# Kernel optimization log

Hardware: AMD Instinct MI355X
Metric: run time of the kernel (lower is better)

## Reference

```python
import jax, jax.numpy as jnp
import numpy as np
import math

HEADS, IN_DIM, OUT_DIM, N = 8, 256, 64, 4096

def _glorot(key, shape):
    fan = shape[-2] + shape[-1]
    lim = math.sqrt(6.0 / fan)
    return jax.random.uniform(key, shape, jnp.float32, -lim, lim)

def setup_inputs() -> dict:
    key = jax.random.key(0)
    ks = jax.random.split(key, 6)
    return {
        "input_x": jax.random.normal(ks[0], (N, IN_DIM), jnp.float32),
        "WQ": _glorot(ks[1], (HEADS, IN_DIM, OUT_DIM)),
        "WK": _glorot(ks[2], (HEADS, IN_DIM, OUT_DIM)),
        "WV": _glorot(ks[3], (HEADS, IN_DIM, OUT_DIM)),
        "lin_w": _glorot(ks[4], (OUT_DIM, HEADS * OUT_DIM)),
        "lin_b": jnp.zeros((OUT_DIM,), jnp.float32),
    }

def reference(input_x, WQ, WK, WV, lin_w, lin_b):
    # Q,K,V: [H, N, D] via broadcasted matmul of [N,in] @ [H,in,D]
    Q = jnp.einsum('ni,hid->hnd', input_x, WQ)
    K = jnp.einsum('ni,hid->hnd', input_x, WK)
    V = jnp.einsum('ni,hid->hnd', input_x, WV)
    scores = jnp.einsum('hnd,hmd->hnm', Q, K)  # [H, N, N]
    # Original adds diag_embed(diag(scores) - 1e20): diagonal -> 2*orig - 1e20
    idx = jnp.arange(scores.shape[-1])
    scores = scores.at[:, idx, idx].add(scores[:, idx, idx] - 1e20)
    attn = jax.nn.softmax(scores / math.sqrt(OUT_DIM), axis=-1)
    attn_x = jnp.einsum('hnm,hmd->hnd', attn, V)  # [H, N, D]
    # cat heads along feature dim: [N, H*D]
    attn_cat = jnp.transpose(attn_x, (1, 0, 2)).reshape(attn_x.shape[1], -1)
    return attn_cat @ lin_w.T + lin_b
```

## Files before the change

kernel.cpp:

```cpp
#include <hip/hip_runtime.h>
#include <hip/hip_bf16.h>

#define SEQ  4096
#define HEADS 8
#define IND  256
#define OUTD 64
#define NSPLIT 4
#define QBLK 128
#define TILES_PER_SLICE (SEQ / 64 / NSPLIT)

typedef __attribute__((ext_vector_type(8))) short bf16x8;
typedef __attribute__((ext_vector_type(4))) float f32x4;

__device__ __forceinline__ unsigned short f2bf(float f) {
  union { __hip_bfloat16 h; unsigned short u; } c;
  c.h = __float2bfloat16(f);
  return c.u;
}
__device__ __forceinline__ float bf2f(unsigned short u) {
  union { unsigned u; float f; } c;
  c.u = ((unsigned)u) << 16;
  return c.f;
}
__device__ __forceinline__ float fast_exp2(float x) {
#if __has_builtin(__builtin_amdgcn_exp2f)
  return __builtin_amdgcn_exp2f(x);
#else
  float r;
  asm("v_exp_f32 %0, %1" : "=v"(r) : "v"(x));
  return r;
#endif
}
__device__ __forceinline__ unsigned pk2(float hi, float lo) {
  return __builtin_amdgcn_perm(__builtin_bit_cast(unsigned, hi),
                               __builtin_bit_cast(unsigned, lo), 0x07060302u);
}
__device__ __forceinline__ int pcol(int k) {
  return (k >> 5) * 32 + ((k >> 2) & 3) * 8 + ((k >> 4) & 1) * 4 + (k & 3);
}

__global__ void prep_kernel(const float* __restrict__ WQ,
                            const float* __restrict__ WK,
                            const float* __restrict__ WV,
                            const float* __restrict__ LW,
                            unsigned short* __restrict__ WTQ,
                            unsigned short* __restrict__ WTK,
                            unsigned short* __restrict__ WTV,
                            unsigned short* __restrict__ LWB) {
  const int NW = HEADS * IND * OUTD;
  const int NL = OUTD * HEADS * OUTD;
  int i = blockIdx.x * 256 + threadIdx.x;
  if (i < 3 * NW) {
    int which = i / NW;
    int r = i % NW;
    int h = r / (IND * OUTD);
    int rem = r % (IND * OUTD);
    int d = rem / IND;
    int ii = rem % IND;
    const float* W = (which == 0) ? WQ : ((which == 1) ? WK : WV);
    float v = W[(h * IND + ii) * OUTD + d];
    if (which == 0) v *= 0.125f * 1.44269504088896f;
    unsigned short* DST = (which == 0) ? WTQ : ((which == 1) ? WTK : WTV);
    DST[h * OUTD * IND + d * IND + ii] = f2bf(v);
  } else if (i < 3 * NW + NL) {
    int k = i - 3 * NW;
    LWB[k] = f2bf(LW[k]);
  }
}

__global__ __launch_bounds__(256) void proj_kernel(
    const float* __restrict__ X,
    const unsigned short* __restrict__ WTQ,
    const unsigned short* __restrict__ WTK,
    const unsigned short* __restrict__ WTV,
    unsigned short* __restrict__ Qo,
    unsigned short* __restrict__ KS,
    unsigned short* __restrict__ VS) {
  const int tb = blockIdx.x;
  const int h  = blockIdx.y;

  __shared__ unsigned short Xl[64 * 72];
  __shared__ unsigned short Wl[3][64 * 72];

  const int tid = threadIdx.x;
  const int lane = tid & 63;
  const int w = tid >> 6;
  const int m16 = lane & 15;
  const int g = lane >> 4;

  const unsigned short* W0 = WTQ + h * OUTD * IND;
  const unsigned short* W1 = WTK + h * OUTD * IND;
  const unsigned short* W2 = WTV + h * OUTD * IND;

  f32x4 acc[3][4];
#pragma unroll
  for (int z = 0; z < 3; ++z)
#pragma unroll
    for (int ns = 0; ns < 4; ++ns) {
      f32x4 z4 = {0.f, 0.f, 0.f, 0.f};
      acc[z][ns] = z4;
    }

  for (int kb = 0; kb < 4; ++kb) {
    if (kb) __syncthreads();
    for (int s = tid; s < 512; s += 256) {
      int row = s >> 3, sg = s & 7;
      const float* xs = X + (size_t)(tb * 64 + row) * IND + kb * 64 + sg * 8;
      float4 x0 = *(const float4*)xs;
      float4 x1 = *(const float4*)(xs + 4);
      uint4 u;
      u.x = ((unsigned)f2bf(x0.y) << 16) | f2bf(x0.x);
      u.y = ((unsigned)f2bf(x0.w) << 16) | f2bf(x0.z);
      u.z = ((unsigned)f2bf(x1.y) << 16) | f2bf(x1.x);
      u.w = ((unsigned)f2bf(x1.w) << 16) | f2bf(x1.z);
      *(uint4*)(&Xl[row * 72 + sg * 8]) = u;
      *(uint4*)(&Wl[0][row * 72 + sg * 8]) =
          *(const uint4*)(W0 + (size_t)row * IND + kb * 64 + sg * 8);
      *(uint4*)(&Wl[1][row * 72 + sg * 8]) =
          *(const uint4*)(W1 + (size_t)row * IND + kb * 64 + sg * 8);
      *(uint4*)(&Wl[2][row * 72 + sg * 8]) =
          *(const uint4*)(W2 + (size_t)row * IND + kb * 64 + sg * 8);
    }
    __syncthreads();
    bf16x8 xa0 = *(const bf16x8*)(&Xl[(w * 16 + m16) * 72 + g * 8]);
    bf16x8 xa1 = *(const bf16x8*)(&Xl[(w * 16 + m16) * 72 + 32 + g * 8]);
#pragma unroll
    for (int z = 0; z < 2; ++z)
#pragma unroll
      for (int ns = 0; ns < 4; ++ns) {
        bf16x8 b0 = *(const bf16x8*)(&Wl[z][(ns * 16 + m16) * 72 + g * 8]);
        bf16x8 b1 = *(const bf16x8*)(&Wl[z][(ns * 16 + m16) * 72 + 32 + g * 8]);
        acc[z][ns] = __builtin_amdgcn_mfma_f32_16x16x32_bf16(xa0, b0, acc[z][ns], 0, 0, 0);
        acc[z][ns] = __builtin_amdgcn_mfma_f32_16x16x32_bf16(xa1, b1, acc[z][ns], 0, 0, 0);
      }
    bf16x8 wa0 = *(const bf16x8*)(&Wl[2][(w * 16 + m16) * 72 + g * 8]);
    bf16x8 wa1 = *(const bf16x8*)(&Wl[2][(w * 16 + m16) * 72 + 32 + g * 8]);
#pragma unroll
    for (int ns = 0; ns < 4; ++ns) {
      bf16x8 b0 = *(const bf16x8*)(&Xl[(ns * 16 + m16) * 72 + g * 8]);
      bf16x8 b1 = *(const bf16x8*)(&Xl[(ns * 16 + m16) * 72 + 32 + g * 8]);
      acc[2][ns] = __builtin_amdgcn_mfma_f32_16x16x32_bf16(wa0, b0, acc[2][ns], 0, 0, 0);
      acc[2][ns] = __builtin_amdgcn_mfma_f32_16x16x32_bf16(wa1, b1, acc[2][ns], 0, 0, 0);
    }
  }
#pragma unroll
  for (int ns = 0; ns < 4; ++ns)
#pragma unroll
    for (int r = 0; r < 4; ++r) {
      int token = tb * 64 + w * 16 + 4 * g + r;
      int d = ns * 16 + m16;
      Qo[(size_t)h * SEQ * OUTD + (size_t)token * OUTD + d] = f2bf(acc[0][ns][r]);
    }
  {
    unsigned short* O = KS + ((size_t)(h * 64 + tb)) * 4096;
#pragma unroll
    for (int ns = 0; ns < 4; ++ns)
#pragma unroll
      for (int r = 0; r < 4; ++r) {
        int rk = w * 16 + 4 * g + r;
        int d = ns * 16 + m16;
        int c = d >> 3;
        int idx = rk * 64 + ((c ^ (rk & 7)) << 3) + (d & 7);
        O[idx] = f2bf(acc[1][ns][r]);
      }
  }
  {
    unsigned short* O = VS + ((size_t)(h * 64 + tb)) * 4096;
#pragma unroll
    for (int ns = 0; ns < 4; ++ns) {
      int cp = pcol(ns * 16 + m16);
      int c = cp >> 3, j = cp & 7;
#pragma unroll
      for (int r = 0; r < 4; ++r) {
        int rv = w * 16 + 4 * g + r;
        int idx = rv * 64 + ((c ^ (rv & 7)) << 3) + j;
        O[idx] = f2bf(acc[2][ns][r]);
      }
    }
  }
}

__global__ __launch_bounds__(256, 4) void attn_kernel(
    const unsigned short* __restrict__ Q,
    const unsigned short* __restrict__ KS,
    const unsigned short* __restrict__ VS,
    unsigned short* __restrict__ PART,
    float* __restrict__ L) {
  const int qb = blockIdx.x;
  const int h  = blockIdx.y;
  const int sl = blockIdx.z;
  const int kb0 = sl * TILES_PER_SLICE;
  const unsigned short* Qh = Q + (size_t)h * SEQ * OUTD;

  __shared__ unsigned short Kl[3][4096];
  __shared__ unsigned short Vl[2][4096];

  const int tid = threadIdx.x;
  const int lane = tid & 63;
  const int w = tid >> 6;
  const int m16 = lane & 15;
  const int g = lane >> 4;
  const int e = m16 & 7;
  const int c0s = ((g ^ e) << 3);
  const int c1s = (((g + 4) ^ e) << 3);

  const int qrowA = qb * QBLK + w * 16 + m16;
  const int qrowB = qrowA + 64;
  bf16x8 qfA0 = *(const bf16x8*)(Qh + (size_t)qrowA * OUTD + g * 8);
  bf16x8 qfA1 = *(const bf16x8*)(Qh + (size_t)qrowA * OUTD + 32 + g * 8);
  bf16x8 qfB0 = *(const bf16x8*)(Qh + (size_t)qrowB * OUTD + g * 8);
  bf16x8 qfB1 = *(const bf16x8*)(Qh + (size_t)qrowB * OUTD + 32 + g * 8);

  f32x4 accA[4], accB[4], acc5A, acc5B;
#pragma unroll
  for (int s4 = 0; s4 < 4; ++s4) {
    f32x4 z4 = {0.f, 0.f, 0.f, 0.f};
    accA[s4] = z4; accB[s4] = z4;
  }
  { f32x4 z4 = {0.f, 0.f, 0.f, 0.f}; acc5A = z4; acc5B = z4; }
  const f32x4 zero4 = {0.f, 0.f, 0.f, 0.f};
  bf16x8 ones;
#pragma unroll
  for (int j = 0; j < 8; ++j) ones[j] = (short)0x3F80;

  const unsigned short* kg = KS + ((size_t)(h * 64 + kb0)) * 4096 + w * 512 + lane * 8;
  const unsigned short* vg = VS + ((size_t)(h * 64 + kb0)) * 4096 + w * 512 + lane * 8;

  auto stageK = [&](int buf) {
    __builtin_amdgcn_global_load_lds(kg, &Kl[buf][w * 512], 16, 0, 0);
    __builtin_amdgcn_global_load_lds(kg + 2048, &Kl[buf][2048 + w * 512], 16, 0, 0);
    kg += 4096;
  };
  auto stageV = [&](int buf) {
    __builtin_amdgcn_global_load_lds(vg, &Vl[buf][w * 512], 16, 0, 0);
    __builtin_amdgcn_global_load_lds(vg + 2048, &Vl[buf][2048 + w * 512], 16, 0, 0);
    vg += 4096;
  };

  stageK(0);
  stageV(0);
  stageK(1);
  asm volatile("s_waitcnt vmcnt(2)" ::: "memory");
  __builtin_amdgcn_s_barrier();
  asm volatile("" ::: "memory");

#pragma unroll
  for (int it = 0; it < TILES_PER_SLICE; ++it) {
    const int kb = kb0 + it;
    const int kcur = it % 3;
    const int vcur = it & 1;
    if (it + 1 < TILES_PER_SLICE) stageV((it + 1) & 1);
    if (it + 2 < TILES_PER_SLICE) stageK((it + 2) % 3);

    f32x4 stA[4], stB[4];
    __builtin_amdgcn_s_setprio(1);
#pragma unroll
    for (int t = 0; t < 4; ++t) {
      const unsigned short* krow = &Kl[kcur][(t * 16 + m16) * 64];
      bf16x8 ka0 = *(const bf16x8*)(krow + c0s);
      bf16x8 ka1 = *(const bf16x8*)(krow + c1s);
      stA[t] = __builtin_amdgcn_mfma_f32_16x16x32_bf16(ka0, qfA0, zero4, 0, 0, 0);
      stA[t] = __builtin_amdgcn_mfma_f32_16x16x32_bf16(ka1, qfA1, stA[t], 0, 0, 0);
      stB[t] = __builtin_amdgcn_mfma_f32_16x16x32_bf16(ka0, qfB0, zero4, 0, 0, 0);
      stB[t] = __builtin_amdgcn_mfma_f32_16x16x32_bf16(ka1, qfB1, stB[t], 0, 0, 0);
    }
    __builtin_amdgcn_s_setprio(0);

    if (kb == 2 * qb) {
#pragma unroll
      for (int t = 0; t < 4; ++t)
#pragma unroll
        for (int r = 0; r < 4; ++r)
          if (t == w && (4 * g + r) == m16) stA[t][r] = -1e30f;
    }
    if (kb == 2 * qb + 1) {
#pragma unroll
      for (int t = 0; t < 4; ++t)
#pragma unroll
        for (int r = 0; r < 4; ++r)
          if (t == w && (4 * g + r) == m16) stB[t][r] = -1e30f;
    }

    float eA[16], eB[16];
#pragma unroll
    for (int t = 0; t < 4; ++t)
#pragma unroll
      for (int r = 0; r < 4; ++r) {
        eA[t * 4 + r] = fast_exp2(stA[t][r]);
        eB[t * 4 + r] = fast_exp2(stB[t][r]);
      }
    uint4 uA0, uA1, uB0, uB1;
    uA0.x = pk2(eA[1], eA[0]);   uA0.y = pk2(eA[3], eA[2]);
    uA0.z = pk2(eA[5], eA[4]);   uA0.w = pk2(eA[7], eA[6]);
    uA1.x = pk2(eA[9], eA[8]);   uA1.y = pk2(eA[11], eA[10]);
    uA1.z = pk2(eA[13], eA[12]); uA1.w = pk2(eA[15], eA[14]);
    uB0.x = pk2(eB[1], eB[0]);   uB0.y = pk2(eB[3], eB[2]);
    uB0.z = pk2(eB[5], eB[4]);   uB0.w = pk2(eB[7], eB[6]);
    uB1.x = pk2(eB[9], eB[8]);   uB1.y = pk2(eB[11], eB[10]);
    uB1.z = pk2(eB[13], eB[12]); uB1.w = pk2(eB[15], eB[14]);
    bf16x8 pbA0 = __builtin_bit_cast(bf16x8, uA0);
    bf16x8 pbA1 = __builtin_bit_cast(bf16x8, uA1);
    bf16x8 pbB0 = __builtin_bit_cast(bf16x8, uB0);
    bf16x8 pbB1 = __builtin_bit_cast(bf16x8, uB1);

    __builtin_amdgcn_s_setprio(1);
#pragma unroll
    for (int s4 = 0; s4 < 4; ++s4) {
      const unsigned short* vrow = &Vl[vcur][(s4 * 16 + m16) * 64];
      bf16x8 va0 = *(const bf16x8*)(vrow + c0s);
      bf16x8 va1 = *(const bf16x8*)(vrow + c1s);
      accA[s4] = __builtin_amdgcn_mfma_f32_16x16x32_bf16(va0, pbA0, accA[s4], 0, 0, 0);
      accA[s4] = __builtin_amdgcn_mfma_f32_16x16x32_bf16(va1, pbA1, accA[s4], 0, 0, 0);
      accB[s4] = __builtin_amdgcn_mfma_f32_16x16x32_bf16(va0, pbB0, accB[s4], 0, 0, 0);
      accB[s4] = __builtin_amdgcn_mfma_f32_16x16x32_bf16(va1, pbB1, accB[s4], 0, 0, 0);
    }
    acc5A = __builtin_amdgcn_mfma_f32_16x16x32_bf16(ones, pbA0, acc5A, 0, 0, 0);
    acc5A = __builtin_amdgcn_mfma_f32_16x16x32_bf16(ones, pbA1, acc5A, 0, 0, 0);
    acc5B = __builtin_amdgcn_mfma_f32_16x16x32_bf16(ones, pbB0, acc5B, 0, 0, 0);
    acc5B = __builtin_amdgcn_mfma_f32_16x16x32_bf16(ones, pbB1, acc5B, 0, 0, 0);
    __builtin_amdgcn_s_setprio(0);

    if (it < TILES_PER_SLICE - 1) {
      if (it < TILES_PER_SLICE - 2) {
        asm volatile("s_waitcnt vmcnt(2)" ::: "memory");
      } else {
        asm volatile("s_waitcnt vmcnt(0)" ::: "memory");
      }
      __builtin_amdgcn_s_barrier();
      asm volatile("" ::: "memory");
    }
  }

  const size_t baseA = (((size_t)sl * HEADS + h) * SEQ + qrowA) * OUTD;
  const size_t baseB = (((size_t)sl * HEADS + h) * SEQ + qrowB) * OUTD;
#pragma unroll
  for (int s4 = 0; s4 < 4; ++s4) {
    uint2 pkA, pkB;
    pkA.x = pk2(accA[s4][1], accA[s4][0]);
    pkA.y = pk2(accA[s4][3], accA[s4][2]);
    pkB.x = pk2(accB[s4][1], accB[s4][0]);
    pkB.y = pk2(accB[s4][3], accB[s4][2]);
    *(uint2*)(&PART[baseA + s4 * 16 + 4 * g]) = pkA;
    *(uint2*)(&PART[baseB + s4 * 16 + 4 * g]) = pkB;
  }
  if (g == 0) {
    L[((size_t)sl * HEADS + h) * SEQ + qrowA] = acc5A[0];
    L[((size_t)sl * HEADS + h) * SEQ + qrowB] = acc5B[0];
  }
}

__global__ __launch_bounds__(128) void final_kernel(
    const unsigned short* __restrict__ PART, const float* __restrict__ L,
    const unsigned short* __restrict__ LWB, const float* __restrict__ LB,
    float* __restrict__ OUT) {
  __shared__ float Rl[64 * 20];
  const int q0 = blockIdx.x * 16;
  const int tid = threadIdx.x;
  const int wv = tid >> 6, lane = tid & 63;
  const int m16 = lane & 15, g = lane >> 4;

  f32x4 acc[4];
#pragma unroll
  for (int ns = 0; ns < 4; ++ns) { f32x4 z4 = {0.f, 0.f, 0.f, 0.f}; acc[ns] = z4; }

#pragma unroll
  for (int kbi = 0; kbi < 4; ++kbi) {
    const int kb = wv * 4 + kbi;
    float lsum = 0.f;
#pragma unroll
    for (int s2 = 0; s2 < NSPLIT; ++s2)
      lsum += L[((size_t)s2 * HEADS + kb) * SEQ + q0 + m16];
    float inv = 1.f / lsum;
    float va[8], vb[8];
#pragma unroll
    for (int j = 0; j < 8; ++j) { va[j] = 0.f; vb[j] = 0.f; }
#pragma unroll
    for (int s2 = 0; s2 < NSPLIT; ++s2) {
      const unsigned short* p =
          PART + (((size_t)s2 * HEADS + kb) * SEQ + q0 + m16) * OUTD;
      bf16x8 t0 = *(const bf16x8*)(p + g * 8);
      bf16x8 t1 = *(const bf16x8*)(p + 32 + g * 8);
#pragma unroll
      for (int j = 0; j < 8; ++j) {
        va[j] += bf2f((unsigned short)t0[j]);
        vb[j] += bf2f((unsigned short)t1[j]);
      }
    }
    uint4 u0, u1;
    u0.x = pk2(va[1] * inv, va[0] * inv); u0.y = pk2(va[3] * inv, va[2] * inv);
    u0.z = pk2(va[5] * inv, va[4] * inv); u0.w = pk2(va[7] * inv, va[6] * inv);
    u1.x = pk2(vb[1] * inv, vb[0] * inv); u1.y = pk2(vb[3] * inv, vb[2] * inv);
    u1.z = pk2(vb[5] * inv, vb[4] * inv); u1.w = pk2(vb[7] * inv, vb[6] * inv);
    bf16x8 a0 = __builtin_bit_cast(bf16x8, u0);
    bf16x8 a1 = __builtin_bit_cast(bf16x8, u1);
#pragma unroll
    for (int ns = 0; ns < 4; ++ns) {
      const unsigned short* lw = LWB + (size_t)(ns * 16 + m16) * 512 + kb * 64;
      bf16x8 b0 = *(const bf16x8*)(lw + g * 8);
      bf16x8 b1 = *(const bf16x8*)(lw + 32 + g * 8);
      acc[ns] = __builtin_amdgcn_mfma_f32_16x16x32_bf16(a0, b0, acc[ns], 0, 0, 0);
      acc[ns] = __builtin_amdgcn_mfma_f32_16x16x32_bf16(a1, b1, acc[ns], 0, 0, 0);
    }
  }

  if (wv == 1) {
#pragma unroll
    for (int ns = 0; ns < 4; ++ns)
      *(f32x4*)(&Rl[lane * 20 + ns * 4]) = acc[ns];
  }
  __syncthreads();
  if (wv == 0) {
#pragma unroll
    for (int ns = 0; ns < 4; ++ns) {
      f32x4 o = acc[ns] + *(const f32x4*)(&Rl[lane * 20 + ns * 4]);
      float b = LB[ns * 16 + m16];
#pragma unroll
      for (int r = 0; r < 4; ++r)
        OUT[(size_t)(q0 + 4 * g + r) * OUTD + ns * 16 + m16] = o[r] + b;
    }
  }
}

extern "C" void kernel_launch(void* const* d_in, const int* in_sizes, int n_in,
                              void* d_out, int out_size, void* d_ws, size_t ws_size,
                              hipStream_t stream) {
  const float* X  = (const float*)d_in[0];
  const float* WQ = (const float*)d_in[1];
  const float* WK = (const float*)d_in[2];
  const float* WV = (const float*)d_in[3];
  const float* LW = (const float*)d_in[4];
  const float* LB = (const float*)d_in[5];

  char* ws = (char*)d_ws;
  unsigned short* Qb  = (unsigned short*)ws;
  unsigned short* KS  = Qb + (size_t)HEADS * SEQ * OUTD;
  unsigned short* VS  = KS + (size_t)HEADS * SEQ * OUTD;
  unsigned short* LWB = VS + (size_t)HEADS * SEQ * OUTD;
  char* region2 = (char*)(LWB + (size_t)OUTD * HEADS * OUTD);

  unsigned short* WTQ = (unsigned short*)region2;
  unsigned short* WTK = WTQ + (size_t)HEADS * OUTD * IND;
  unsigned short* WTV = WTK + (size_t)HEADS * OUTD * IND;

  unsigned short* PART = (unsigned short*)region2;
  float* Lml = (float*)(region2 + (size_t)NSPLIT * HEADS * SEQ * OUTD * 2);

  const int total_prep = 3 * HEADS * IND * OUTD + OUTD * HEADS * OUTD;
  prep_kernel<<<(total_prep + 255) / 256, 256, 0, stream>>>(
      WQ, WK, WV, LW, WTQ, WTK, WTV, LWB);
  proj_kernel<<<dim3(64, 8), 256, 0, stream>>>(X, WTQ, WTK, WTV, Qb, KS, VS);
  attn_kernel<<<dim3(SEQ / QBLK, 8, NSPLIT), 256, 0, stream>>>(Qb, KS, VS, PART, Lml);
  final_kernel<<<256, 128, 0, stream>>>(PART, Lml, LWB, LB, (float*)d_out);
}
```

Measured before the change: 66.29 us.

## Software-pipeline QK and PV across tiles; widen final kernel to four waves

The attention loop is restructured so that each iteration's QK MFMAs are issued alongside the previous tile's PV MFMAs, with exp/pack moved after them and the last PV step peeled out of the loop. The aim is to overlap the exp/transcendental work with matrix-core work instead of serialising them. V staging is shifted by one tile to match the new ordering. The final kernel also moves from two to four waves per block, each handling two heads, with a three-way LDS reduction. This adds register pressure from the live P fragments across iterations and changes the timing of the waits.

```diff
diff --git a/kernel.cpp b/kernel.cpp
--- a/kernel.cpp
+++ b/kernel.cpp
@@ -237,22 +237,10 @@
     vg += 4096;
   };
 
-  stageK(0);
-  stageV(0);
-  stageK(1);
-  asm volatile("s_waitcnt vmcnt(2)" ::: "memory");
-  __builtin_amdgcn_s_barrier();
-  asm volatile("" ::: "memory");
-
-#pragma unroll
-  for (int it = 0; it < TILES_PER_SLICE; ++it) {
-    const int kb = kb0 + it;
-    const int kcur = it % 3;
-    const int vcur = it & 1;
-    if (it + 1 < TILES_PER_SLICE) stageV((it + 1) & 1);
-    if (it + 2 < TILES_PER_SLICE) stageK((it + 2) % 3);
-
-    f32x4 stA[4], stB[4];
+  bf16x8 pbA0, pbA1, pbB0, pbB1;
+  f32x4 stA[4], stB[4];
+
+  auto qk_mfma = [&](int kcur) {
     __builtin_amdgcn_s_setprio(1);
 #pragma unroll
     for (int t = 0; t < 4; ++t) {
@@ -265,22 +253,42 @@
       stB[t] = __builtin_amdgcn_mfma_f32_16x16x32_bf16(ka1, qfB1, stB[t], 0, 0, 0);
     }
     __builtin_amdgcn_s_setprio(0);
-
-    if (kb == 2 * qb) {
+  };
+
+  auto pv_step = [&](int vbuf) {
+    __builtin_amdgcn_s_setprio(1);
+#pragma unroll
+    for (int s4 = 0; s4 < 4; ++s4) {
+      const unsigned short* vrow = &Vl[vbuf][(s4 * 16 + m16) * 64];
+      bf16x8 va0 = *(const bf16x8*)(vrow + c0s);
+      bf16x8 va1 = *(const bf16x8*)(vrow + c1s);
+      accA[s4] = __builtin_amdgcn_mfma_f32_16x16x32_bf16(va0, pbA0, accA[s4], 0, 0, 0);
+      accA[s4] = __builtin_amdgcn_mfma_f32_16x16x32_bf16(va1, pbA1, accA[s4], 0, 0, 0);
+      accB[s4] = __builtin_amdgcn_mfma_f32_16x16x32_bf16(va0, pbB0, accB[s4], 0, 0, 0);
+      accB[s4] = __builtin_amdgcn_mfma_f32_16x16x32_bf16(va1, pbB1, accB[s4], 0, 0, 0);
+    }
+    acc5A = __builtin_amdgcn_mfma_f32_16x16x32_bf16(ones, pbA0, acc5A, 0, 0, 0);
+    acc5A = __builtin_amdgcn_mfma_f32_16x16x32_bf16(ones, pbA1, acc5A, 0, 0, 0);
+    acc5B = __builtin_amdgcn_mfma_f32_16x16x32_bf16(ones, pbB0, acc5B, 0, 0, 0);
+    acc5B = __builtin_amdgcn_mfma_f32_16x16x32_bf16(ones, pbB1, acc5B, 0, 0, 0);
+    __builtin_amdgcn_s_setprio(0);
+  };
+
+  auto mask_pack = [&](int kbg) {
+    if (kbg == 2 * qb) {
 #pragma unroll
       for (int t = 0; t < 4; ++t)
 #pragma unroll
         for (int r = 0; r < 4; ++r)
           if (t == w && (4 * g + r) == m16) stA[t][r] = -1e30f;
     }
-    if (kb == 2 * qb + 1) {
+    if (kbg == 2 * qb + 1) {
 #pragma unroll
       for (int t = 0; t < 4; ++t)
 #pragma unroll
         for (int r = 0; r < 4; ++r)
           if (t == w && (4 * g + r) == m16) stB[t][r] = -1e30f;
     }
-
     float eA[16], eB[16];
 #pragma unroll
     for (int t = 0; t < 4; ++t)
@@ -298,27 +306,27 @@
     uB0.z = pk2(eB[5], eB[4]);   uB0.w = pk2(eB[7], eB[6]);
     uB1.x = pk2(eB[9], eB[8]);   uB1.y = pk2(eB[11], eB[10]);
     uB1.z = pk2(eB[13], eB[12]); uB1.w = pk2(eB[15], eB[14]);
-    bf16x8 pbA0 = __builtin_bit_cast(bf16x8, uA0);
-    bf16x8 pbA1 = __builtin_bit_cast(bf16x8, uA1);
-    bf16x8 pbB0 = __builtin_bit_cast(bf16x8, uB0);
-    bf16x8 pbB1 = __builtin_bit_cast(bf16x8, uB1);
-
-    __builtin_amdgcn_s_setprio(1);
-#pragma unroll
-    for (int s4 = 0; s4 < 4; ++s4) {
-      const unsigned short* vrow = &Vl[vcur][(s4 * 16 + m16) * 64];
-      bf16x8 va0 = *(const bf16x8*)(vrow + c0s);
-      bf16x8 va1 = *(const bf16x8*)(vrow + c1s);
-      accA[s4] = __builtin_amdgcn_mfma_f32_16x16x32_bf16(va0, pbA0, accA[s4], 0, 0, 0);
-      accA[s4] = __builtin_amdgcn_mfma_f32_16x16x32_bf16(va1, pbA1, accA[s4], 0, 0, 0);
-      accB[s4] = __builtin_amdgcn_mfma_f32_16x16x32_bf16(va0, pbB0, accB[s4], 0, 0, 0);
-      accB[s4] = __builtin_amdgcn_mfma_f32_16x16x32_bf16(va1, pbB1, accB[s4], 0, 0, 0);
-    }
-    acc5A = __builtin_amdgcn_mfma_f32_16x16x32_bf16(ones, pbA0, acc5A, 0, 0, 0);
-    acc5A = __builtin_amdgcn_mfma_f32_16x16x32_bf16(ones, pbA1, acc5A, 0, 0, 0);
-    acc5B = __builtin_amdgcn_mfma_f32_16x16x32_bf16(ones, pbB0, acc5B, 0, 0, 0);
-    acc5B = __builtin_amdgcn_mfma_f32_16x16x32_bf16(ones, pbB1, acc5B, 0, 0, 0);
-    __builtin_amdgcn_s_setprio(0);
+    pbA0 = __builtin_bit_cast(bf16x8, uA0);
+    pbA1 = __builtin_bit_cast(bf16x8, uA1);
+    pbB0 = __builtin_bit_cast(bf16x8, uB0);
+    pbB1 = __builtin_bit_cast(bf16x8, uB1);
+  };
+
+  stageK(0);
+  stageK(1);
+  asm volatile("s_waitcnt vmcnt(2)" ::: "memory");
+  __builtin_amdgcn_s_barrier();
+  asm volatile("" ::: "memory");
+
+#pragma unroll
+  for (int it = 0; it < TILES_PER_SLICE; ++it) {
+    if (it < TILES_PER_SLICE) stageV(it & 1);
+    if (it + 2 < TILES_PER_SLICE) stageK((it + 2) % 3);
+
+    qk_mfma(it % 3);
+    if (it > 0) pv_step((it - 1) & 1);
+
+    mask_pack(kb0 + it);
 
     if (it < TILES_PER_SLICE - 1) {
       if (it < TILES_PER_SLICE - 2) {
@@ -330,6 +338,10 @@
       asm volatile("" ::: "memory");
     }
   }
+  asm volatile("s_waitcnt vmcnt(0)" ::: "memory");
+  __builtin_amdgcn_s_barrier();
+  asm volatile("" ::: "memory");
+  pv_step((TILES_PER_SLICE - 1) & 1);
 
   const size_t baseA = (((size_t)sl * HEADS + h) * SEQ + qrowA) * OUTD;
   const size_t baseB = (((size_t)sl * HEADS + h) * SEQ + qrowB) * OUTD;
@@ -349,11 +361,11 @@
   }
 }
 
-__global__ __launch_bounds__(128) void final_kernel(
+__global__ __launch_bounds__(256) void final_kernel(
     const unsigned short* __restrict__ PART, const float* __restrict__ L,
     const unsigned short* __restrict__ LWB, const float* __restrict__ LB,
     float* __restrict__ OUT) {
-  __shared__ float Rl[64 * 20];
+  __shared__ float Rl[3][64 * 20];
   const int q0 = blockIdx.x * 16;
   const int tid = threadIdx.x;
   const int wv = tid >> 6, lane = tid & 63;
@@ -364,8 +376,8 @@
   for (int ns = 0; ns < 4; ++ns) { f32x4 z4 = {0.f, 0.f, 0.f, 0.f}; acc[ns] = z4; }
 
 #pragma unroll
-  for (int kbi = 0; kbi < 4; ++kbi) {
-    const int kb = wv * 4 + kbi;
+  for (int kbi = 0; kbi < 2; ++kbi) {
+    const int kb = wv * 2 + kbi;
     float lsum = 0.f;
 #pragma unroll
     for (int s2 = 0; s2 < NSPLIT; ++s2)
@@ -403,16 +415,19 @@
     }
   }
 
-  if (wv == 1) {
+  if (wv != 0) {
 #pragma unroll
     for (int ns = 0; ns < 4; ++ns)
-      *(f32x4*)(&Rl[lane * 20 + ns * 4]) = acc[ns];
+      *(f32x4*)(&Rl[wv - 1][lane * 20 + ns * 4]) = acc[ns];
   }
   __syncthreads();
   if (wv == 0) {
 #pragma unroll
     for (int ns = 0; ns < 4; ++ns) {
-      f32x4 o = acc[ns] + *(const f32x4*)(&Rl[lane * 20 + ns * 4]);
+      f32x4 o = acc[ns];
+#pragma unroll
+      for (int rr = 0; rr < 3; ++rr)
+        o += *(const f32x4*)(&Rl[rr][lane * 20 + ns * 4]);
       float b = LB[ns * 16 + m16];
 #pragma unroll
       for (int r = 0; r < 4; ++r)
@@ -450,5 +465,5 @@
       WQ, WK, WV, LW, WTQ, WTK, WTV, LWB);
   proj_kernel<<<dim3(64, 8), 256, 0, stream>>>(X, WTQ, WTK, WTV, Qb, KS, VS);
   attn_kernel<<<dim3(SEQ / QBLK, 8, NSPLIT), 256, 0, stream>>>(Qb, KS, VS, PART, Lml);
-  final_kernel<<<256, 128, 0, stream>>>(PART, Lml, LWB, LB, (float*)d_out);
-}
+  final_kernel<<<256, 256, 0, stream>>>(PART, Lml, LWB, LB, (float*)d_out);
+}
```

After: 67.89 us. +2.4%, slower.

## Split attention warps across query and key halves with LDS reduction, three KV slices

Applied to the files above, without the earlier changes.

Restructures the attention kernel so each warp pair covers 64 query rows and half of each 64-key tile. This lets the ones-vector MFMA row-sum be replaced by a VALU sum of bf16-truncated exponentials. The two key halves are reduced through LDS at the end, and the KV split drops from 4 to 3 uneven slices (22/21/21 tiles) with launch bounds lowered to 3. The aim is to cut redundant MFMA work and fit the grid to the CU count, at the cost of an extra LDS reduction and a non-unrolled loop.

```diff
diff --git a/kernel.cpp b/kernel.cpp
--- a/kernel.cpp
+++ b/kernel.cpp
@@ -5,9 +5,8 @@
 #define HEADS 8
 #define IND  256
 #define OUTD 64
-#define NSPLIT 4
+#define NSPLIT 3
 #define QBLK 128
-#define TILES_PER_SLICE (SEQ / 64 / NSPLIT)
 
 typedef __attribute__((ext_vector_type(8))) short bf16x8;
 typedef __attribute__((ext_vector_type(4))) float f32x4;
@@ -30,6 +29,9 @@
   asm("v_exp_f32 %0, %1" : "=v"(r) : "v"(x));
   return r;
 #endif
+}
+__device__ __forceinline__ float trunc_bf(float x) {
+  return __builtin_bit_cast(float, __builtin_bit_cast(unsigned, x) & 0xffff0000u);
 }
 __device__ __forceinline__ unsigned pk2(float hi, float lo) {
   return __builtin_amdgcn_perm(__builtin_bit_cast(unsigned, hi),
@@ -180,7 +182,7 @@
   }
 }
 
-__global__ __launch_bounds__(256, 4) void attn_kernel(
+__global__ __launch_bounds__(256, 3) void attn_kernel(
     const unsigned short* __restrict__ Q,
     const unsigned short* __restrict__ KS,
     const unsigned short* __restrict__ VS,
@@ -189,39 +191,41 @@
   const int qb = blockIdx.x;
   const int h  = blockIdx.y;
   const int sl = blockIdx.z;
-  const int kb0 = sl * TILES_PER_SLICE;
-  const unsigned short* Qh = Q + (size_t)h * SEQ * OUTD;
+  const int kb0 = (sl == 0) ? 0 : (22 + 21 * (sl - 1));
+  const int len = (sl == 0) ? 22 : 21;
 
   __shared__ unsigned short Kl[3][4096];
   __shared__ unsigned short Vl[2][4096];
+  __shared__ float Lred[2][64];
 
   const int tid = threadIdx.x;
   const int lane = tid & 63;
   const int w = tid >> 6;
+  const int qh = w >> 1;
+  const int kh = w & 1;
   const int m16 = lane & 15;
   const int g = lane >> 4;
   const int e = m16 & 7;
-  const int c0s = ((g ^ e) << 3);
-  const int c1s = (((g + 4) ^ e) << 3);
-
-  const int qrowA = qb * QBLK + w * 16 + m16;
-  const int qrowB = qrowA + 64;
-  bf16x8 qfA0 = *(const bf16x8*)(Qh + (size_t)qrowA * OUTD + g * 8);
-  bf16x8 qfA1 = *(const bf16x8*)(Qh + (size_t)qrowA * OUTD + 32 + g * 8);
-  bf16x8 qfB0 = *(const bf16x8*)(Qh + (size_t)qrowB * OUTD + g * 8);
-  bf16x8 qfB1 = *(const bf16x8*)(Qh + (size_t)qrowB * OUTD + 32 + g * 8);
-
-  f32x4 accA[4], accB[4], acc5A, acc5B;
-#pragma unroll
-  for (int s4 = 0; s4 < 4; ++s4) {
-    f32x4 z4 = {0.f, 0.f, 0.f, 0.f};
-    accA[s4] = z4; accB[s4] = z4;
-  }
-  { f32x4 z4 = {0.f, 0.f, 0.f, 0.f}; acc5A = z4; acc5B = z4; }
+
+  const unsigned short* Qh = Q + ((size_t)h * SEQ + qb * QBLK + qh * 64) * OUTD;
+  bf16x8 qf[2][4];
+#pragma unroll
+  for (int c = 0; c < 2; ++c)
+#pragma unroll
+    for (int j = 0; j < 4; ++j)
+      qf[c][j] = *(const bf16x8*)(Qh + (size_t)(j * 16 + m16) * OUTD + c * 32 + g * 8);
+
+  f32x4 acc[4][4];
+#pragma unroll
+  for (int ds = 0; ds < 4; ++ds)
+#pragma unroll
+    for (int j = 0; j < 4; ++j) {
+      f32x4 z4 = {0.f, 0.f, 0.f, 0.f};
+      acc[ds][j] = z4;
+    }
+  float lp[4] = {0.f, 0.f, 0.f, 0.f};
+  bf16x8 pb[4];
   const f32x4 zero4 = {0.f, 0.f, 0.f, 0.f};
-  bf16x8 ones;
-#pragma unroll
-  for (int j = 0; j < 8; ++j) ones[j] = (short)0x3F80;
 
   const unsigned short* kg = KS + ((size_t)(h * 64 + kb0)) * 4096 + w * 512 + lane * 8;
   const unsigned short* vg = VS + ((size_t)(h * 64 + kb0)) * 4096 + w * 512 + lane * 8;
@@ -244,84 +248,73 @@
   __builtin_amdgcn_s_barrier();
   asm volatile("" ::: "memory");
 
-#pragma unroll
-  for (int it = 0; it < TILES_PER_SLICE; ++it) {
-    const int kb = kb0 + it;
-    const int kcur = it % 3;
-    const int vcur = it & 1;
-    if (it + 1 < TILES_PER_SLICE) stageV((it + 1) & 1);
-    if (it + 2 < TILES_PER_SLICE) stageK((it + 2) % 3);
-
-    f32x4 stA[4], stB[4];
-    __builtin_amdgcn_s_setprio(1);
-#pragma unroll
-    for (int t = 0; t < 4; ++t) {
-      const unsigned short* krow = &Kl[kcur][(t * 16 + m16) * 64];
-      bf16x8 ka0 = *(const bf16x8*)(krow + c0s);
-      bf16x8 ka1 = *(const bf16x8*)(krow + c1s);
-      stA[t] = __builtin_amdgcn_mfma_f32_16x16x32_bf16(ka0, qfA0, zero4, 0, 0, 0);
-      stA[t] = __builtin_amdgcn_mfma_f32_16x16x32_bf16(ka1, qfA1, stA[t], 0, 0, 0);
-      stB[t] = __builtin_amdgcn_mfma_f32_16x16x32_bf16(ka0, qfB0, zero4, 0, 0, 0);
-      stB[t] = __builtin_amdgcn_mfma_f32_16x16x32_bf16(ka1, qfB1, stB[t], 0, 0, 0);
-    }
-    __builtin_amdgcn_s_setprio(0);
-
-    if (kb == 2 * qb) {
-#pragma unroll
-      for (int t = 0; t < 4; ++t)
-#pragma unroll
-        for (int r = 0; r < 4; ++r)
-          if (t == w && (4 * g + r) == m16) stA[t][r] = -1e30f;
-    }
-    if (kb == 2 * qb + 1) {
-#pragma unroll
-      for (int t = 0; t < 4; ++t)
-#pragma unroll
-        for (int r = 0; r < 4; ++r)
-          if (t == w && (4 * g + r) == m16) stB[t][r] = -1e30f;
-    }
-
-    float eA[16], eB[16];
-#pragma unroll
-    for (int t = 0; t < 4; ++t)
-#pragma unroll
-      for (int r = 0; r < 4; ++r) {
-        eA[t * 4 + r] = fast_exp2(stA[t][r]);
-        eB[t * 4 + r] = fast_exp2(stB[t][r]);
-      }
-    uint4 uA0, uA1, uB0, uB1;
-    uA0.x = pk2(eA[1], eA[0]);   uA0.y = pk2(eA[3], eA[2]);
-    uA0.z = pk2(eA[5], eA[4]);   uA0.w = pk2(eA[7], eA[6]);
-    uA1.x = pk2(eA[9], eA[8]);   uA1.y = pk2(eA[11], eA[10]);
-    uA1.z = pk2(eA[13], eA[12]); uA1.w = pk2(eA[15], eA[14]);
-    uB0.x = pk2(eB[1], eB[0]);   uB0.y = pk2(eB[3], eB[2]);
-    uB0.z = pk2(eB[5], eB[4]);   uB0.w = pk2(eB[7], eB[6]);
-    uB1.x = pk2(eB[9], eB[8]);   uB1.y = pk2(eB[11], eB[10]);
-    uB1.z = pk2(eB[13], eB[12]); uB1.w = pk2(eB[15], eB[14]);
-    bf16x8 pbA0 = __builtin_bit_cast(bf16x8, uA0);
-    bf16x8 pbA1 = __builtin_bit_cast(bf16x8, uA1);
-    bf16x8 pbB0 = __builtin_bit_cast(bf16x8, uB0);
-    bf16x8 pbB1 = __builtin_bit_cast(bf16x8, uB1);
-
-    __builtin_amdgcn_s_setprio(1);
-#pragma unroll
-    for (int s4 = 0; s4 < 4; ++s4) {
-      const unsigned short* vrow = &Vl[vcur][(s4 * 16 + m16) * 64];
-      bf16x8 va0 = *(const bf16x8*)(vrow + c0s);
-      bf16x8 va1 = *(const bf16x8*)(vrow + c1s);
-      accA[s4] = __builtin_amdgcn_mfma_f32_16x16x32_bf16(va0, pbA0, accA[s4], 0, 0, 0);
-      accA[s4] = __builtin_amdgcn_mfma_f32_16x16x32_bf16(va1, pbA1, accA[s4], 0, 0, 0);
-      accB[s4] = __builtin_amdgcn_mfma_f32_16x16x32_bf16(va0, pbB0, accB[s4], 0, 0, 0);
-      accB[s4] = __builtin_amdgcn_mfma_f32_16x16x32_bf16(va1, pbB1, accB[s4], 0, 0, 0);
-    }
-    acc5A = __builtin_amdgcn_mfma_f32_16x16x32_bf16(ones, pbA0, acc5A, 0, 0, 0);
-    acc5A = __builtin_amdgcn_mfma_f32_16x16x32_bf16(ones, pbA1, acc5A, 0, 0, 0);
-    acc5B = __builtin_amdgcn_mfma_f32_16x16x32_bf16(ones, pbB0, acc5B, 0, 0, 0);
-    acc5B = __builtin_amdgcn_mfma_f32_16x16x32_bf16(ones, pbB1, acc5B, 0, 0, 0);
-    __builtin_amdgcn_s_setprio(0);
-
-    if (it < TILES_PER_SLICE - 1) {
-      if (it < TILES_PER_SLICE - 2) {
+  int ck = 0;
+  int kn = 2;
+  for (int it = 0; it < len; ++it) {
+    const int cv = it & 1;
+    if (it + 1 < len) stageV((it + 1) & 1);
+    if (it + 2 < len) { stageK(kn); kn = (kn == 2) ? 0 : kn + 1; }
+
+    {
+      const unsigned short* Kb_ = &Kl[ck][0];
+      bf16x8 ka[2][2];
+#pragma unroll
+      for (int kt = 0; kt < 2; ++kt) {
+        const unsigned short* krow = Kb_ + (kh * 32 + kt * 16 + m16) * 64;
+        ka[kt][0] = *(const bf16x8*)(krow + ((g ^ e) << 3));
+        ka[kt][1] = *(const bf16x8*)(krow + (((4 + g) ^ e) << 3));
+      }
+      const bool dg = (kb0 + it) == (2 * qb + qh);
+      __builtin_amdgcn_s_setprio(1);
+#pragma unroll
+      for (int j = 0; j < 4; ++j) {
+        f32x4 s0 = __builtin_amdgcn_mfma_f32_16x16x32_bf16(ka[0][0], qf[0][j], zero4, 0, 0, 0);
+        s0 = __builtin_amdgcn_mfma_f32_16x16x32_bf16(ka[0][1], qf[1][j], s0, 0, 0, 0);
+        f32x4 s1 = __builtin_amdgcn_mfma_f32_16x16x32_bf16(ka[1][0], qf[0][j], zero4, 0, 0, 0);
+        s1 = __builtin_amdgcn_mfma_f32_16x16x32_bf16(ka[1][1], qf[1][j], s1, 0, 0, 0);
+        if (dg && j == kh * 2) {
+#pragma unroll
+          for (int r = 0; r < 4; ++r)
+            if (4 * g + r == m16) s0[r] = -1e30f;
+        }
+        if (dg && j == kh * 2 + 1) {
+#pragma unroll
+          for (int r = 0; r < 4; ++r)
+            if (4 * g + r == m16) s1[r] = -1e30f;
+        }
+        float e0 = fast_exp2(s0[0]), e1 = fast_exp2(s0[1]);
+        float e2 = fast_exp2(s0[2]), e3 = fast_exp2(s0[3]);
+        float e4 = fast_exp2(s1[0]), e5 = fast_exp2(s1[1]);
+        float e6 = fast_exp2(s1[2]), e7 = fast_exp2(s1[3]);
+        uint4 u;
+        u.x = pk2(e1, e0);
+        u.y = pk2(e3, e2);
+        u.z = pk2(e5, e4);
+        u.w = pk2(e7, e6);
+        pb[j] = __builtin_bit_cast(bf16x8, u);
+        lp[j] += ((trunc_bf(e0) + trunc_bf(e1)) + (trunc_bf(e2) + trunc_bf(e3))) +
+                 ((trunc_bf(e4) + trunc_bf(e5)) + (trunc_bf(e6) + trunc_bf(e7)));
+      }
+      __builtin_amdgcn_s_setprio(0);
+    }
+
+    {
+      const unsigned short* Vb_ = &Vl[cv][0];
+      __builtin_amdgcn_s_setprio(1);
+#pragma unroll
+      for (int ds = 0; ds < 4; ++ds) {
+        const unsigned short* vrow = Vb_ + (ds * 16 + m16) * 64;
+        bf16x8 va = *(const bf16x8*)(vrow + (((kh * 4 + g) ^ e) << 3));
+#pragma unroll
+        for (int j = 0; j < 4; ++j)
+          acc[ds][j] = __builtin_amdgcn_mfma_f32_16x16x32_bf16(va, pb[j], acc[ds][j], 0, 0, 0);
+      }
+      __builtin_amdgcn_s_setprio(0);
+    }
+
+    ck = (ck == 2) ? 0 : ck + 1;
+    if (it < len - 1) {
+      if (it < len - 2) {
         asm volatile("s_waitcnt vmcnt(2)" ::: "memory");
       } else {
         asm volatile("s_waitcnt vmcnt(0)" ::: "memory");
@@ -331,21 +324,48 @@
     }
   }
 
-  const size_t baseA = (((size_t)sl * HEADS + h) * SEQ + qrowA) * OUTD;
-  const size_t baseB = (((size_t)sl * HEADS + h) * SEQ + qrowB) * OUTD;
-#pragma unroll
-  for (int s4 = 0; s4 < 4; ++s4) {
-    uint2 pkA, pkB;
-    pkA.x = pk2(accA[s4][1], accA[s4][0]);
-    pkA.y = pk2(accA[s4][3], accA[s4][2]);
-    pkB.x = pk2(accB[s4][1], accB[s4][0]);
-    pkB.y = pk2(accB[s4][3], accB[s4][2]);
-    *(uint2*)(&PART[baseA + s4 * 16 + 4 * g]) = pkA;
-    *(uint2*)(&PART[baseB + s4 * 16 + 4 * g]) = pkB;
-  }
-  if (g == 0) {
-    L[((size_t)sl * HEADS + h) * SEQ + qrowA] = acc5A[0];
-    L[((size_t)sl * HEADS + h) * SEQ + qrowB] = acc5B[0];
+#pragma unroll
+  for (int j = 0; j < 4; ++j) {
+    lp[j] += __shfl_xor(lp[j], 16);
+    lp[j] += __shfl_xor(lp[j], 32);
+  }
+
+  __syncthreads();
+  float* Red = (float*)&Kl[0][0];
+  if (kh == 1) {
+    float* R = Red + qh * 4096;
+#pragma unroll
+    for (int ds = 0; ds < 4; ++ds)
+#pragma unroll
+      for (int j = 0; j < 4; ++j) {
+        int u = (ds * 4 + g) ^ m16;
+        *(f32x4*)(R + (j * 16 + m16) * 64 + u * 4) = acc[ds][j];
+      }
+    if (g == 0) {
+#pragma unroll
+      for (int j = 0; j < 4; ++j) Lred[qh][j * 16 + m16] = lp[j];
+    }
+  }
+  __syncthreads();
+  if (kh == 0) {
+    const float* R = Red + qh * 4096;
+    const size_t prow = ((size_t)sl * HEADS + h) * SEQ + qb * QBLK + qh * 64;
+#pragma unroll
+    for (int ds = 0; ds < 4; ++ds)
+#pragma unroll
+      for (int j = 0; j < 4; ++j) {
+        int u = (ds * 4 + g) ^ m16;
+        f32x4 o = acc[ds][j] + *(const f32x4*)(R + (j * 16 + m16) * 64 + u * 4);
+        uint2 pk;
+        pk.x = pk2(o[1], o[0]);
+        pk.y = pk2(o[3], o[2]);
+        *(uint2*)(&PART[(prow + j * 16 + m16) * OUTD + ds * 16 + 4 * g]) = pk;
+      }
+    if (g == 0) {
+#pragma unroll
+      for (int j = 0; j < 4; ++j)
+        L[prow + j * 16 + m16] = lp[j] + Lred[qh][j * 16 + m16];
+    }
   }
 }
 
@@ -449,6 +469,7 @@
   prep_kernel<<<(total_prep + 255) / 256, 256, 0, stream>>>(
       WQ, WK, WV, LW, WTQ, WTK, WTV, LWB);
   proj_kernel<<<dim3(64, 8), 256, 0, stream>>>(X, WTQ, WTK, WTV, Qb, KS, VS);
-  attn_kernel<<<dim3(SEQ / QBLK, 8, NSPLIT), 256, 0, stream>>>(Qb, KS, VS, PART, Lml);
+  attn_kernel<<<dim3(SEQ / QBLK, HEADS, NSPLIT), 256, 0, stream>>>(
+      Qb, KS, VS, PART, Lml);
   final_kernel<<<256, 128, 0, stream>>>(PART, Lml, LWB, LB, (float*)d_out);
 }
```

Measured after the change: 75.37 us. 13.7% more time.
